# Performance work log

Hardware: AMD Instinct MI355X
Metric: run time of the kernel (lower is better)

The kernel has to match this reference:

```python
import jax, jax.numpy as jnp
import numpy as np

B, S, H = 64, 512, 768
A1, C1 = 100, 300          # token-attention and sentence-classifier hidden sizes
BETA = 1.0                 # soft_attention_beta
SLW, TLW, RLW = 1.0, 1.0, 0.01  # loss weights


def setup_inputs() -> dict:
    key = jax.random.key(0)
    ks = jax.random.split(key, 12)
    hidden_states = jax.random.normal(ks[0], (B, S, H), jnp.float32)
    # token_attention: Linear(H,100) -> Tanh -> Linear(100,1) -> Sigmoid
    w1 = jax.random.normal(ks[1], (H, A1), jnp.float32) * 0.02
    b1 = jnp.zeros((A1,), jnp.float32)
    w2 = jax.random.normal(ks[2], (A1, 1), jnp.float32) * 0.02
    b2 = jnp.zeros((1,), jnp.float32)
    # sentence_classification: Linear(H,300) -> Tanh -> Linear(300,1) -> Sigmoid
    sw1 = jax.random.normal(ks[3], (H, C1), jnp.float32) * 0.02
    sb1 = jnp.zeros((C1,), jnp.float32)
    sw2 = jax.random.normal(ks[4], (C1, 1), jnp.float32) * 0.02
    sb2 = jnp.zeros((1,), jnp.float32)
    offset_mapping = jax.random.randint(ks[5], (B, S, 2), 0, 4).astype(jnp.int32)
    offset_mapping = offset_mapping.at[:, 0, 0].set(0)  # first token starts a word
    # labels in {-1, 0, 1}; -1 = ignore
    labels = jax.random.randint(ks[6], (B, S), -1, 2).astype(jnp.float32)
    return {
        "hidden_states": hidden_states,
        "w1": w1, "b1": b1, "w2": w2, "b2": b2,
        "sw1": sw1, "sb1": sb1, "sw2": sw2, "sb2": sb2,
        "labels": labels,
        "offset_mapping": offset_mapping,
    }


def _forward(hidden_states, w1, b1, w2, b2, sw1, sb1, sw2, sb2, labels, offset_mapping):
    # token attention scores in (0,1): [B, S]
    token_att = jax.nn.sigmoid(
        jnp.tanh(hidden_states @ w1 + b1) @ w2 + b2
    )[..., 0]

    # ragged per-word subword max-pooling (segment-max along the sequence)
    not_subword = offset_mapping[:, :, 0] == 0                 # [B, S] word starts
    seg = jnp.maximum(jnp.cumsum(not_subword.astype(jnp.int32), axis=1) - 1, 0)

    def _seg_max(vals, seg_ids):
        return jax.ops.segment_max(vals, seg_ids, num_segments=S)

    segmax = jax.vmap(_seg_max)(token_att, seg)                # [B, S] per-word max
    word_att = jnp.where(not_subword, jnp.take_along_axis(segmax, seg, axis=1), 0.0)

    # mask: labeled tokens that are word starts
    token_mask = ((labels != -1) & not_subword).astype(token_att.dtype)
    masked = word_att * token_mask                              # token_logits [B, S]

    # beta-normalized soft attention pooling over hidden states
    p = masked ** BETA
    att_norm = p / jnp.sum(p, axis=1, keepdims=True)            # [B, S]
    pooled = jnp.einsum("bsh,bs->bh", hidden_states, att_norm)  # [B, H]

    sent = jax.nn.sigmoid(jnp.tanh(pooled @ sw1 + sb1) @ sw2 + sb2)  # [B, 1]

    # losses (MSE with reduction='sum')
    sentence_labels = jnp.max(labels, axis=1, keepdims=True)    # [B, 1]
    sentence_loss = jnp.sum((sent - sentence_labels) ** 2)
    zero_labels = jnp.where(labels != -1, labels, 0.0)
    token_loss = jnp.sum((masked - zero_labels) ** 2)
    ones_masked = jnp.where(masked == 0, 1.0, masked)
    reg_a = jnp.sum(jnp.min(ones_masked, axis=1, keepdims=True) ** 2)
    reg_b = jnp.sum((jnp.max(masked, axis=1, keepdims=True) - sentence_labels) ** 2)
    total = SLW * sentence_loss + TLW * token_loss + RLW * (reg_a + reg_b)
    return total, sentence_loss, token_loss, reg_a, reg_b, masked, sent


def reference(hidden_states, w1, b1, w2, b2, sw1, sb1, sw2, sb2, labels, offset_mapping):
    return _forward(hidden_states, w1, b1, w2, b2, sw1, sb1, sw2, sb2,
                    labels, offset_mapping)
```

## Files before the change

kernel.cpp:

```cpp
#include <hip/hip_runtime.h>
#include <math.h>

#define BB 64
#define SS 512
#define HH 768
#define AA1 100
#define CC1 300

typedef __bf16 bf16x8 __attribute__((ext_vector_type(8)));
typedef float f32x4 __attribute__((ext_vector_type(4)));

#ifndef __has_builtin
#define __has_builtin(x) 0
#endif
#if __has_builtin(__builtin_amdgcn_global_load_lds)
#define HAVE_GLL 1
#else
#define HAVE_GLL 0
#endif

#define AS1 __attribute__((address_space(1)))
#define AS3 __attribute__((address_space(3)))

__global__ __launch_bounds__(256) void k_prep(const float* __restrict__ w1,
                                              __bf16* __restrict__ w1i) {
    int idx = blockIdx.x * 256 + threadIdx.x;
    int j = idx % 112;
    int r = idx / 112;
    int e = r & 7, g = r >> 3;
    int k = (g >> 2) * 32 + (g & 3) * 8 + e;
    float v = (j < AA1) ? w1[k * AA1 + j] : 0.f;
    w1i[((size_t)g * 112 + j) * 8 + e] = (__bf16)v;
}

__global__ __launch_bounds__(256) void k_token_att(
        const float* __restrict__ hs, const __bf16* __restrict__ w1i,
        const float* __restrict__ b1, const float* __restrict__ w2,
        const float* __restrict__ b2, float* __restrict__ token_att) {
    const int tid = threadIdx.x;
    const int tok0 = blockIdx.x * 64;
    const int w = tid >> 6, lane = tid & 63;
    const int q = lane >> 4, ln = lane & 15;
    const int trow = tok0 + w * 16 + ln;

    f32x4 acc[7];
#pragma unroll
    for (int n = 0; n < 7; n++) acc[n] = (f32x4){0.f, 0.f, 0.f, 0.f};

    const float* ga = hs + (size_t)trow * HH + q * 8;
    const __bf16* gb = w1i + (size_t)(q * 112 + ln) * 8;

#pragma unroll 4
    for (int kt = 0; kt < 24; kt++) {
        f32x4 a0 = *(const f32x4*)(ga + kt * 32);
        f32x4 a1 = *(const f32x4*)(ga + kt * 32 + 4);
        bf16x8 af;
#pragma unroll
        for (int e = 0; e < 4; e++) {
            af[e] = (__bf16)a0[e];
            af[e + 4] = (__bf16)a1[e];
        }
        const __bf16* gbk = gb + (size_t)kt * 3584;
#pragma unroll
        for (int n = 0; n < 7; n++) {
            bf16x8 bf = *(const bf16x8*)(gbk + n * 128);
            acc[n] = __builtin_amdgcn_mfma_f32_16x16x32_bf16(af, bf, acc[n], 0, 0, 0);
        }
    }

    float s0 = 0.f, s1 = 0.f, s2 = 0.f, s3 = 0.f;
#pragma unroll
    for (int n = 0; n < 7; n++) {
        int j = n * 16 + ln;
        if (j < AA1) {
            float bj = b1[j], wj = w2[j];
            s0 += tanhf(acc[n][0] + bj) * wj;
            s1 += tanhf(acc[n][1] + bj) * wj;
            s2 += tanhf(acc[n][2] + bj) * wj;
            s3 += tanhf(acc[n][3] + bj) * wj;
        }
    }
#pragma unroll
    for (int off = 1; off < 16; off <<= 1) {
        s0 += __shfl_xor(s0, off); s1 += __shfl_xor(s1, off);
        s2 += __shfl_xor(s2, off); s3 += __shfl_xor(s3, off);
    }
    if (ln == 0) {
        float bb = b2[0];
        int base = tok0 + w * 16 + q * 4;
        token_att[base + 0] = 1.f / (1.f + expf(-(s0 + bb)));
        token_att[base + 1] = 1.f / (1.f + expf(-(s1 + bb)));
        token_att[base + 2] = 1.f / (1.f + expf(-(s2 + bb)));
        token_att[base + 3] = 1.f / (1.f + expf(-(s3 + bb)));
    }
}

__global__ __launch_bounds__(512) void k_mask(
        const float* __restrict__ token_att, const float* __restrict__ labels,
        const int* __restrict__ offm, float* __restrict__ masked_out,
        float* __restrict__ cw_g, short* __restrict__ cs_g,
        int* __restrict__ nnz_g, float* __restrict__ inv_g,
        float4* __restrict__ stats_g) {
    __shared__ int smax[512];
    __shared__ int wscan[8];
    __shared__ int wscan2[8];
    __shared__ float wred[5][8];

    const int b = blockIdx.x, s = threadIdx.x;
    const int lane = s & 63, wv = s >> 6;
    const int ns = (offm[(b * SS + s) * 2] == 0) ? 1 : 0;

    int v = ns;
#pragma unroll
    for (int off = 1; off < 64; off <<= 1) {
        int o = __shfl_up(v, off);
        if (lane >= off) v += o;
    }
    if (lane == 63) wscan[wv] = v;
    smax[s] = 0;
    __syncthreads();
    int woff = 0;
    for (int i = 0; i < 8; i++) woff += (i < wv) ? wscan[i] : 0;
    const int seg = max(v + woff - 1, 0);

    const float ta = token_att[b * SS + s];
    atomicMax(&smax[seg], __float_as_int(ta));
    __syncthreads();

    const float wa = ns ? __int_as_float(smax[seg]) : 0.f;
    const float lab = labels[b * SS + s];
    const float m = (lab != -1.f && ns) ? wa : 0.f;
    masked_out[b * SS + s] = m;

    const float zl = (lab != -1.f) ? lab : 0.f;
    const float tl = (m - zl) * (m - zl);
    const float ones = (m == 0.f) ? 1.f : m;

    float r0 = m, r1 = tl, r2 = m, r3 = ones, r4 = lab;
#pragma unroll
    for (int off = 32; off > 0; off >>= 1) {
        r0 += __shfl_xor(r0, off);
        r1 += __shfl_xor(r1, off);
        r2 = fmaxf(r2, __shfl_xor(r2, off));
        r3 = fminf(r3, __shfl_xor(r3, off));
        r4 = fmaxf(r4, __shfl_xor(r4, off));
    }
    if (lane == 0) {
        wred[0][wv] = r0; wred[1][wv] = r1; wred[2][wv] = r2;
        wred[3][wv] = r3; wred[4][wv] = r4;
    }

    const int nz = (m != 0.f) ? 1 : 0;
    int v2 = nz;
#pragma unroll
    for (int off = 1; off < 64; off <<= 1) {
        int o = __shfl_up(v2, off);
        if (lane >= off) v2 += o;
    }
    if (lane == 63) wscan2[wv] = v2;
    __syncthreads();

    int woff2 = 0;
    for (int i = 0; i < 8; i++) woff2 += (i < wv) ? wscan2[i] : 0;
    if (nz) {
        int pos = v2 + woff2 - 1;
        cw_g[b * SS + pos] = m;
        cs_g[b * SS + pos] = (short)s;
    }
    if (s == 0) {
        float att = 0.f, tokl = 0.f, maxm = -1e30f, minone = 1e30f, slab = -1e30f;
        int nnz = 0;
        for (int i = 0; i < 8; i++) {
            att += wred[0][i]; tokl += wred[1][i];
            maxm = fmaxf(maxm, wred[2][i]);
            minone = fminf(minone, wred[3][i]);
            slab = fmaxf(slab, wred[4][i]);
            nnz += wscan2[i];
        }
        nnz_g[b] = nnz;
        inv_g[b] = 1.f / att;
        stats_g[b] = make_float4(tokl, maxm, minone, slab);
    }
}

__global__ __launch_bounds__(256) void k_pool(
        const float* __restrict__ hs, const float* __restrict__ cw_g,
        const short* __restrict__ cs_g, const int* __restrict__ nnz_g,
        const float* __restrict__ inv_g, float* __restrict__ pooled,
        float* __restrict__ zsum) {
    __shared__ float wl[SS];
    __shared__ short il[SS];
    __shared__ float red[256];

    const int b = blockIdx.x, hc = blockIdx.y;
    const int tid = threadIdx.x;
    const int nnz = nnz_g[b];
    if (hc == 0 && tid == 0) zsum[b] = 0.f;
    if (tid < nnz) { wl[tid] = cw_g[b * SS + tid]; il[tid] = cs_g[b * SS + tid]; }
    if (tid + 256 < nnz) {
        wl[tid + 256] = cw_g[b * SS + tid + 256];
        il[tid + 256] = cs_g[b * SS + tid + 256];
    }
    __syncthreads();

    const int h = (tid & 63) + hc * 64;
    const int slot = tid >> 6;
    const float* hsb = hs + (size_t)b * SS * HH + h;
    const int len = (nnz + 3) >> 2;
    const int i0 = slot * len;
    const int i1 = min(i0 + len, nnz);
    float a0 = 0.f, a1 = 0.f, a2 = 0.f, a3 = 0.f;
    int i = i0;
    for (; i + 4 <= i1; i += 4) {
        a0 += hsb[(size_t)il[i]     * HH] * wl[i];
        a1 += hsb[(size_t)il[i + 1] * HH] * wl[i + 1];
        a2 += hsb[(size_t)il[i + 2] * HH] * wl[i + 2];
        a3 += hsb[(size_t)il[i + 3] * HH] * wl[i + 3];
    }
    for (; i < i1; i++) a0 += hsb[(size_t)il[i] * HH] * wl[i];
    red[tid] = (a0 + a1) + (a2 + a3);
    __syncthreads();
    if (tid < 64)
        pooled[(size_t)b * HH + h] =
            (red[tid] + red[tid + 64] + red[tid + 128] + red[tid + 192]) * inv_g[b];
}

__global__ __launch_bounds__(256) void k_sent(
        const float* __restrict__ pooled, const float* __restrict__ sw1,
        const float* __restrict__ sb1, const float* __restrict__ sw2,
        float* __restrict__ zsum) {
    __shared__ float pl[HH];
    __shared__ float red[256];

    const int b = blockIdx.x, cc = blockIdx.y;
    const int tid = threadIdx.x;
    pl[tid]       = pooled[(size_t)b * HH + tid];
    pl[tid + 256] = pooled[(size_t)b * HH + tid + 256];
    pl[tid + 512] = pooled[(size_t)b * HH + tid + 512];
    __syncthreads();

    const int cl = tid & 63, kq = tid >> 6;
    const int c = cc * 60 + cl;
    float z = 0.f;
    if (cl < 60) {
        const int k0 = kq * 192;
        for (int k = k0; k < k0 + 192; k += 8) {
#pragma unroll
            for (int u = 0; u < 8; u++)
                z += pl[k + u] * sw1[(size_t)(k + u) * CC1 + c];
        }
    }
    red[tid] = z;
    __syncthreads();
    if (kq == 0) {
        float zz = red[tid] + red[tid + 64] + red[tid + 128] + red[tid + 192];
        float t = 0.f;
        if (cl < 60) t = tanhf(zz + sb1[c]) * sw2[c];
#pragma unroll
        for (int off = 32; off > 0; off >>= 1) t += __shfl_xor(t, off);
        if (cl == 0) atomicAdd(&zsum[b], t);
    }
}

__global__ __launch_bounds__(64) void k_losses(
        const float* __restrict__ zsum, const float* __restrict__ sb2,
        const float4* __restrict__ stats_g, float* __restrict__ sent_out,
        float* __restrict__ out) {
    const int b = threadIdx.x;
    const float sv = 1.f / (1.f + expf(-(zsum[b] + sb2[0])));
    sent_out[b] = sv;
    const float4 st = stats_g[b];
    float vs = sv - st.w; vs *= vs;
    float ra = st.z * st.z;
    float rb = st.y - st.w; rb *= rb;
    float s0 = vs, s1 = st.x, s2 = ra, s3 = rb;
#pragma unroll
    for (int off = 32; off > 0; off >>= 1) {
        s0 += __shfl_xor(s0, off);
        s1 += __shfl_xor(s1, off);
        s2 += __shfl_xor(s2, off);
        s3 += __shfl_xor(s3, off);
    }
    if (b == 0) {
        out[1] = s0; out[2] = s1; out[3] = s2; out[4] = s3;
        out[0] = s0 + s1 + 0.01f * (s2 + s3);
    }
}

extern "C" void kernel_launch(void* const* d_in, const int* in_sizes, int n_in,
                              void* d_out, int out_size, void* d_ws, size_t ws_size,
                              hipStream_t stream) {
    const float* hs  = (const float*)d_in[0];
    const float* w1  = (const float*)d_in[1];
    const float* b1  = (const float*)d_in[2];
    const float* w2  = (const float*)d_in[3];
    const float* b2  = (const float*)d_in[4];
    const float* sw1 = (const float*)d_in[5];
    const float* sb1 = (const float*)d_in[6];
    const float* sw2 = (const float*)d_in[7];
    const float* sb2 = (const float*)d_in[8];
    const float* labels = (const float*)d_in[9];
    const int*   offm   = (const int*)d_in[10];

    float* out = (float*)d_out;
    float* ws  = (float*)d_ws;

    float*  token_att = ws;
    __bf16* w1i    = (__bf16*)(ws + 32768);
    float*  cw     = ws + 32768 + 43008;
    short*  cs     = (short*)(cw + 32768);
    int*    nnz    = (int*)(cw + 32768 + 16384);
    float*  inv    = (float*)(nnz + 64);
    float4* stats  = (float4*)(inv + 64);
    float*  pooled = ws;
    float*  zsum   = ws + 49152;

    float* masked_out = out + 5;
    float* sent_out   = out + 5 + BB * SS;

    hipLaunchKernelGGL(k_prep, dim3(336), dim3(256), 0, stream, w1, w1i);
    hipLaunchKernelGGL(k_token_att, dim3(512), dim3(256), 0, stream,
                       hs, w1i, b1, w2, b2, token_att);
    hipLaunchKernelGGL(k_mask, dim3(BB), dim3(512), 0, stream,
                       token_att, labels, offm, masked_out,
                       cw, cs, nnz, inv, stats);
    hipLaunchKernelGGL(k_pool, dim3(BB, 12), dim3(256), 0, stream,
                       hs, cw, cs, nnz, inv, pooled, zsum);
    hipLaunchKernelGGL(k_sent, dim3(BB, 5), dim3(256), 0, stream,
                       pooled, sw1, sb1, sw2, zsum);
    hipLaunchKernelGGL(k_losses, dim3(1), dim3(64), 0, stream,
                       zsum, sb2, stats, sent_out, out);
}
```

Before: 209.0 us.

## Fuse mask into pooling and loss into sentence kernel via last-block counter

The per-batch mask/segment-max/compaction work is recomputed redundantly inside each of the 12 pooling blocks, so the compacted weights stay in shared memory instead of going through global memory. The final loss reduction is folded into the sentence-classifier kernel using an atomic completion counter, so the last block computes the losses. Two kernel launches and their global round-trips are removed. In exchange, the mask work is duplicated twelvefold and the design depends on threadfence/atomic ordering for correctness.

```diff
diff --git a/kernel.cpp b/kernel.cpp
--- a/kernel.cpp
+++ b/kernel.cpp
@@ -9,18 +9,6 @@
 
 typedef __bf16 bf16x8 __attribute__((ext_vector_type(8)));
 typedef float f32x4 __attribute__((ext_vector_type(4)));
-
-#ifndef __has_builtin
-#define __has_builtin(x) 0
-#endif
-#if __has_builtin(__builtin_amdgcn_global_load_lds)
-#define HAVE_GLL 1
-#else
-#define HAVE_GLL 0
-#endif
-
-#define AS1 __attribute__((address_space(1)))
-#define AS3 __attribute__((address_space(3)))
 
 __global__ __launch_bounds__(256) void k_prep(const float* __restrict__ w1,
                                               __bf16* __restrict__ w1i) {
@@ -95,48 +83,71 @@
     }
 }
 
-__global__ __launch_bounds__(512) void k_mask(
-        const float* __restrict__ token_att, const float* __restrict__ labels,
-        const int* __restrict__ offm, float* __restrict__ masked_out,
-        float* __restrict__ cw_g, short* __restrict__ cs_g,
-        int* __restrict__ nnz_g, float* __restrict__ inv_g,
-        float4* __restrict__ stats_g) {
-    __shared__ int smax[512];
-    __shared__ int wscan[8];
-    __shared__ int wscan2[8];
-    __shared__ float wred[5][8];
-
-    const int b = blockIdx.x, s = threadIdx.x;
-    const int lane = s & 63, wv = s >> 6;
-    const int ns = (offm[(b * SS + s) * 2] == 0) ? 1 : 0;
-
-    int v = ns;
+__global__ __launch_bounds__(256) void k_poolmask(
+        const float* __restrict__ hs, const float* __restrict__ token_att,
+        const float* __restrict__ labels, const int* __restrict__ offm,
+        float* __restrict__ masked_out, float* __restrict__ pooled,
+        float4* __restrict__ stats_g, float* __restrict__ zsum,
+        int* __restrict__ cnt2) {
+    __shared__ int smax[SS];
+    __shared__ float wl[SS];
+    __shared__ short il[SS];
+    __shared__ float red[256];
+    __shared__ int wscan[4];
+    __shared__ int wscan2[4];
+    __shared__ float wred[5][4];
+    __shared__ float sh_inv;
+    __shared__ int sh_nnz;
+
+    const int b = blockIdx.x, hc = blockIdx.y;
+    const int t = threadIdx.x;
+    const int lane = t & 63, wv = t >> 6;
+    const int s0 = 2 * t, s1 = s0 + 1;
+
+    const int4 om = ((const int4*)offm)[b * 256 + t];
+    const int ns0 = (om.x == 0) ? 1 : 0;
+    const int ns1 = (om.z == 0) ? 1 : 0;
+
+    int v = ns0 + ns1;
 #pragma unroll
     for (int off = 1; off < 64; off <<= 1) {
         int o = __shfl_up(v, off);
         if (lane >= off) v += o;
     }
     if (lane == 63) wscan[wv] = v;
-    smax[s] = 0;
+    smax[s0] = 0;
+    smax[s1] = 0;
     __syncthreads();
     int woff = 0;
-    for (int i = 0; i < 8; i++) woff += (i < wv) ? wscan[i] : 0;
-    const int seg = max(v + woff - 1, 0);
-
-    const float ta = token_att[b * SS + s];
-    atomicMax(&smax[seg], __float_as_int(ta));
-    __syncthreads();
-
-    const float wa = ns ? __int_as_float(smax[seg]) : 0.f;
-    const float lab = labels[b * SS + s];
-    const float m = (lab != -1.f && ns) ? wa : 0.f;
-    masked_out[b * SS + s] = m;
-
-    const float zl = (lab != -1.f) ? lab : 0.f;
-    const float tl = (m - zl) * (m - zl);
-    const float ones = (m == 0.f) ? 1.f : m;
-
-    float r0 = m, r1 = tl, r2 = m, r3 = ones, r4 = lab;
+    for (int i = 0; i < 4; i++) woff += (i < wv) ? wscan[i] : 0;
+    const int cum1 = v + woff;
+    const int cum0 = cum1 - ns1;
+    const int seg0 = max(cum0 - 1, 0);
+    const int seg1 = max(cum1 - 1, 0);
+
+    const float2 ta = ((const float2*)token_att)[b * 256 + t];
+    atomicMax(&smax[seg0], __float_as_int(ta.x));
+    atomicMax(&smax[seg1], __float_as_int(ta.y));
+    __syncthreads();
+
+    const float2 lab = ((const float2*)labels)[b * 256 + t];
+    const float wa0 = ns0 ? __int_as_float(smax[seg0]) : 0.f;
+    const float wa1 = ns1 ? __int_as_float(smax[seg1]) : 0.f;
+    const float m0 = (lab.x != -1.f && ns0) ? wa0 : 0.f;
+    const float m1 = (lab.y != -1.f && ns1) ? wa1 : 0.f;
+    if (hc == 0) {
+        masked_out[b * SS + s0] = m0;
+        masked_out[b * SS + s1] = m1;
+    }
+    const float zl0 = (lab.x != -1.f) ? lab.x : 0.f;
+    const float zl1 = (lab.y != -1.f) ? lab.y : 0.f;
+    const float tl0 = (m0 - zl0) * (m0 - zl0);
+    const float tl1 = (m1 - zl1) * (m1 - zl1);
+    const float on0 = (m0 == 0.f) ? 1.f : m0;
+    const float on1 = (m1 == 0.f) ? 1.f : m1;
+
+    float r0 = m0 + m1, r1 = tl0 + tl1;
+    float r2 = fmaxf(m0, m1), r3 = fminf(on0, on1), r4 = fmaxf(lab.x, lab.y);
 #pragma unroll
     for (int off = 32; off > 0; off >>= 1) {
         r0 += __shfl_xor(r0, off);
@@ -150,8 +161,9 @@
         wred[3][wv] = r3; wred[4][wv] = r4;
     }
 
-    const int nz = (m != 0.f) ? 1 : 0;
-    int v2 = nz;
+    const int nz0 = (m0 != 0.f) ? 1 : 0;
+    const int nz1 = (m1 != 0.f) ? 1 : 0;
+    int v2 = nz0 + nz1;
 #pragma unroll
     for (int off = 1; off < 64; off <<= 1) {
         int o = __shfl_up(v2, off);
@@ -159,52 +171,36 @@
     }
     if (lane == 63) wscan2[wv] = v2;
     __syncthreads();
-
     int woff2 = 0;
-    for (int i = 0; i < 8; i++) woff2 += (i < wv) ? wscan2[i] : 0;
-    if (nz) {
-        int pos = v2 + woff2 - 1;
-        cw_g[b * SS + pos] = m;
-        cs_g[b * SS + pos] = (short)s;
-    }
-    if (s == 0) {
+    for (int i = 0; i < 4; i++) woff2 += (i < wv) ? wscan2[i] : 0;
+    const int incl = v2 + woff2;
+    if (nz1) { wl[incl - 1] = m1; il[incl - 1] = (short)s1; }
+    if (nz0) { wl[incl - 1 - nz1] = m0; il[incl - 1 - nz1] = (short)s0; }
+
+    if (t == 0) {
         float att = 0.f, tokl = 0.f, maxm = -1e30f, minone = 1e30f, slab = -1e30f;
-        int nnz = 0;
-        for (int i = 0; i < 8; i++) {
+        int nz = 0;
+        for (int i = 0; i < 4; i++) {
             att += wred[0][i]; tokl += wred[1][i];
             maxm = fmaxf(maxm, wred[2][i]);
             minone = fminf(minone, wred[3][i]);
             slab = fmaxf(slab, wred[4][i]);
-            nnz += wscan2[i];
-        }
-        nnz_g[b] = nnz;
-        inv_g[b] = 1.f / att;
-        stats_g[b] = make_float4(tokl, maxm, minone, slab);
-    }
-}
-
-__global__ __launch_bounds__(256) void k_pool(
-        const float* __restrict__ hs, const float* __restrict__ cw_g,
-        const short* __restrict__ cs_g, const int* __restrict__ nnz_g,
-        const float* __restrict__ inv_g, float* __restrict__ pooled,
-        float* __restrict__ zsum) {
-    __shared__ float wl[SS];
-    __shared__ short il[SS];
-    __shared__ float red[256];
-
-    const int b = blockIdx.x, hc = blockIdx.y;
-    const int tid = threadIdx.x;
-    const int nnz = nnz_g[b];
-    if (hc == 0 && tid == 0) zsum[b] = 0.f;
-    if (tid < nnz) { wl[tid] = cw_g[b * SS + tid]; il[tid] = cs_g[b * SS + tid]; }
-    if (tid + 256 < nnz) {
-        wl[tid + 256] = cw_g[b * SS + tid + 256];
-        il[tid + 256] = cs_g[b * SS + tid + 256];
-    }
-    __syncthreads();
-
-    const int h = (tid & 63) + hc * 64;
-    const int slot = tid >> 6;
+            nz += wscan2[i];
+        }
+        sh_inv = 1.f / att;
+        sh_nnz = nz;
+        if (hc == 0) {
+            stats_g[b] = make_float4(tokl, maxm, minone, slab);
+            zsum[b] = 0.f;
+            if (b == 0) *cnt2 = 0;
+        }
+    }
+    __syncthreads();
+
+    const int nnz = sh_nnz;
+    const float inv = sh_inv;
+    const int h = (t & 63) + hc * 64;
+    const int slot = t >> 6;
     const float* hsb = hs + (size_t)b * SS * HH + h;
     const int len = (nnz + 3) >> 2;
     const int i0 = slot * len;
@@ -218,19 +214,22 @@
         a3 += hsb[(size_t)il[i + 3] * HH] * wl[i + 3];
     }
     for (; i < i1; i++) a0 += hsb[(size_t)il[i] * HH] * wl[i];
-    red[tid] = (a0 + a1) + (a2 + a3);
-    __syncthreads();
-    if (tid < 64)
+    red[t] = (a0 + a1) + (a2 + a3);
+    __syncthreads();
+    if (t < 64)
         pooled[(size_t)b * HH + h] =
-            (red[tid] + red[tid + 64] + red[tid + 128] + red[tid + 192]) * inv_g[b];
-}
-
-__global__ __launch_bounds__(256) void k_sent(
+            (red[t] + red[t + 64] + red[t + 128] + red[t + 192]) * inv;
+}
+
+__global__ __launch_bounds__(256) void k_sentloss(
         const float* __restrict__ pooled, const float* __restrict__ sw1,
         const float* __restrict__ sb1, const float* __restrict__ sw2,
-        float* __restrict__ zsum) {
+        const float* __restrict__ sb2, const float4* __restrict__ stats_g,
+        float* __restrict__ zsum, int* __restrict__ cnt2,
+        float* __restrict__ sent_out, float* __restrict__ out) {
     __shared__ float pl[HH];
     __shared__ float red[256];
+    __shared__ int lastF;
 
     const int b = blockIdx.x, cc = blockIdx.y;
     const int tid = threadIdx.x;
@@ -254,36 +253,43 @@
     __syncthreads();
     if (kq == 0) {
         float zz = red[tid] + red[tid + 64] + red[tid + 128] + red[tid + 192];
-        float t = 0.f;
-        if (cl < 60) t = tanhf(zz + sb1[c]) * sw2[c];
-#pragma unroll
-        for (int off = 32; off > 0; off >>= 1) t += __shfl_xor(t, off);
-        if (cl == 0) atomicAdd(&zsum[b], t);
-    }
-}
-
-__global__ __launch_bounds__(64) void k_losses(
-        const float* __restrict__ zsum, const float* __restrict__ sb2,
-        const float4* __restrict__ stats_g, float* __restrict__ sent_out,
-        float* __restrict__ out) {
-    const int b = threadIdx.x;
-    const float sv = 1.f / (1.f + expf(-(zsum[b] + sb2[0])));
-    sent_out[b] = sv;
-    const float4 st = stats_g[b];
-    float vs = sv - st.w; vs *= vs;
-    float ra = st.z * st.z;
-    float rb = st.y - st.w; rb *= rb;
-    float s0 = vs, s1 = st.x, s2 = ra, s3 = rb;
-#pragma unroll
-    for (int off = 32; off > 0; off >>= 1) {
-        s0 += __shfl_xor(s0, off);
-        s1 += __shfl_xor(s1, off);
-        s2 += __shfl_xor(s2, off);
-        s3 += __shfl_xor(s3, off);
-    }
-    if (b == 0) {
-        out[1] = s0; out[2] = s1; out[3] = s2; out[4] = s3;
-        out[0] = s0 + s1 + 0.01f * (s2 + s3);
+        float tt = 0.f;
+        if (cl < 60) tt = tanhf(zz + sb1[c]) * sw2[c];
+#pragma unroll
+        for (int off = 32; off > 0; off >>= 1) tt += __shfl_xor(tt, off);
+        if (cl == 0) atomicAdd(&zsum[b], tt);
+    }
+    __syncthreads();
+
+    if (tid == 0) {
+        __threadfence();
+        int old = atomicAdd(cnt2, 1);
+        lastF = (old == BB * 5 - 1) ? 1 : 0;
+    }
+    __syncthreads();
+    if (!lastF) return;
+    __threadfence();
+
+    if (tid < 64) {
+        const float zs = atomicAdd(&zsum[tid], 0.f);
+        const float sv = 1.f / (1.f + expf(-(zs + sb2[0])));
+        sent_out[tid] = sv;
+        const float4 st = stats_g[tid];
+        float vs = sv - st.w; vs *= vs;
+        float ra = st.z * st.z;
+        float rb = st.y - st.w; rb *= rb;
+        float s0 = vs, s1 = st.x, s2 = ra, s3 = rb;
+#pragma unroll
+        for (int off = 32; off > 0; off >>= 1) {
+            s0 += __shfl_xor(s0, off);
+            s1 += __shfl_xor(s1, off);
+            s2 += __shfl_xor(s2, off);
+            s3 += __shfl_xor(s3, off);
+        }
+        if (tid == 0) {
+            out[1] = s0; out[2] = s1; out[3] = s2; out[4] = s3;
+            out[0] = s0 + s1 + 0.01f * (s2 + s3);
+        }
     }
 }
 
@@ -307,13 +313,10 @@
 
     float*  token_att = ws;
     __bf16* w1i    = (__bf16*)(ws + 32768);
-    float*  cw     = ws + 32768 + 43008;
-    short*  cs     = (short*)(cw + 32768);
-    int*    nnz    = (int*)(cw + 32768 + 16384);
-    float*  inv    = (float*)(nnz + 64);
-    float4* stats  = (float4*)(inv + 64);
-    float*  pooled = ws;
-    float*  zsum   = ws + 49152;
+    float*  pooled = ws + 75776;
+    float*  zsum   = ws + 124928;
+    float4* stats  = (float4*)(ws + 124992);
+    int*    cnt2   = (int*)(ws + 125248);
 
     float* masked_out = out + 5;
     float* sent_out   = out + 5 + BB * SS;
@@ -321,13 +324,10 @@
     hipLaunchKernelGGL(k_prep, dim3(336), dim3(256), 0, stream, w1, w1i);
     hipLaunchKernelGGL(k_token_att, dim3(512), dim3(256), 0, stream,
                        hs, w1i, b1, w2, b2, token_att);
-    hipLaunchKernelGGL(k_mask, dim3(BB), dim3(512), 0, stream,
-                       token_att, labels, offm, masked_out,
-                       cw, cs, nnz, inv, stats);
-    hipLaunchKernelGGL(k_pool, dim3(BB, 12), dim3(256), 0, stream,
-                       hs, cw, cs, nnz, inv, pooled, zsum);
-    hipLaunchKernelGGL(k_sent, dim3(BB, 5), dim3(256), 0, stream,
-                       pooled, sw1, sb1, sw2, zsum);
-    hipLaunchKernelGGL(k_losses, dim3(1), dim3(64), 0, stream,
-                       zsum, sb2, stats, sent_out, out);
-}
+    hipLaunchKernelGGL(k_poolmask, dim3(BB, 12), dim3(256), 0, stream,
+                       hs, token_att, labels, offm, masked_out,
+                       pooled, stats, zsum, cnt2);
+    hipLaunchKernelGGL(k_sentloss, dim3(BB, 5), dim3(256), 0, stream,
+                       pooled, sw1, sb1, sw2, sb2, stats, zsum, cnt2,
+                       sent_out, out);
+}
```

After: 209.8 us. Within noise of the previous version (+0.4%).
